# Kernel tuning notes

Hardware: AMD Instinct MI355X
Metric: run time of the kernel (lower is better)

Reference implementation:

```python
import jax, jax.numpy as jnp
import numpy as np

B, L, D = 8, 1024, 1024  # L must equal D for the elementwise sqrt(K) divide to broadcast


def setup_inputs() -> dict:
    key = jax.random.key(0)
    ks = jax.random.split(key, 9)
    # Non-negative inputs/weights/biases so K = x @ Wk.T + bk >= 0 and sqrt(K) is finite.
    rc = jax.random.uniform(ks[0], (B, L, D), dtype=jnp.float32)
    ri = jax.random.uniform(ks[1], (B, L, D), dtype=jnp.float32)
    tc = jax.random.uniform(ks[2], (B, L, D), dtype=jnp.float32)
    scale = 0.02
    Wq = jax.random.uniform(ks[3], (D, D), dtype=jnp.float32) * scale
    Wk = jax.random.uniform(ks[4], (D, D), dtype=jnp.float32) * scale
    Wv = jax.random.uniform(ks[5], (D, D), dtype=jnp.float32) * scale
    bq = jax.random.uniform(ks[6], (D,), dtype=jnp.float32) * scale
    bk = jax.random.uniform(ks[7], (D,), dtype=jnp.float32) * scale
    bv = jax.random.uniform(ks[8], (D,), dtype=jnp.float32) * scale
    return {
        "reference_caption": rc,
        "reference_image": ri,
        "target_caption": tc,
        "Wq": Wq, "bq": bq,
        "Wk": Wk, "bk": bk,
        "Wv": Wv, "bv": bv,
    }


def reference(reference_caption, reference_image, target_caption, Wq, bq, Wk, bk, Wv, bv):
    # torch nn.Linear: y = x @ W.T + b
    Q = reference_caption @ Wq.T + bq          # [B, Lq, D]
    K = reference_image @ Wk.T + bk            # [B, Lk, D]
    V = reference_image @ Wv.T + bv            # [B, Lk, D]
    matmul_qk = jnp.einsum("bqd,bkd->bqk", Q, K)  # [B, Lq, Lk]
    # Faithful to source: elementwise divide by sqrt(K) tensor (broadcasts since Lq==Lk==D).
    scaled_logits = matmul_qk / jnp.sqrt(K)
    attention_weights = jax.nn.softmax(scaled_logits, axis=-1)
    output = jnp.einsum("bqk,bkd->bqd", attention_weights, V)
    return (output, attention_weights)
```

## Files before the change

kernel.cpp:

```cpp
#include <hip/hip_runtime.h>
#include <hip/hip_fp16.h>
#include <math.h>

typedef unsigned short u16;
typedef __attribute__((ext_vector_type(8))) _Float16 half8;
typedef __attribute__((ext_vector_type(4))) float f32x4;

#define ASLOT 4096
#define SLOT  12288

__device__ __forceinline__ u16 f2h(float f){ __half h=__float2half(f); u16 r; __builtin_memcpy(&r,&h,2); return r; }
__device__ __forceinline__ float h2f(u16 u){ __half h; __builtin_memcpy(&h,&u,2); return __half2float(h); }

template<int ROWS>
__device__ __forceinline__ void stage_tile(const u16* __restrict__ G, int rowbase, int ldg,
                                           int k0, u16* Ls, int tid){
#pragma unroll
    for (int p = 0; p < ROWS / 64; ++p){
        const int lin = tid + p * 256;
        const int row = lin >> 2;
        const int cg  = ((lin & 3) ^ ((row >> 1) & 3)) * 8;
        const u16* g = G + (size_t)(rowbase + row) * ldg + (k0 + cg);
        __builtin_amdgcn_global_load_lds(
            (__attribute__((address_space(1))) void*)g,
            (__attribute__((address_space(3))) void*)(Ls + (size_t)lin * 8), 16, 0, 0);
    }
}

template<int EPI, int BIASM>
__device__ __forceinline__ void gemm_core(
    const u16* __restrict__ A, const u16* __restrict__ B,
    const float* __restrict__ bias,
    float* __restrict__ of, u16* __restrict__ oh,
    const float* __restrict__ cm, u16* __restrict__ od,
    int by, int bx, int lda, int ldb, int ldc, int K, u16* sh)
{
    const int tid  = threadIdx.x;
    const int lane = tid & 63, wv = tid >> 6;
    const int wr = (wv >> 1) * 64;
    const int wc = (wv & 1) * 128;
    const int row0 = by * 128, col0 = bx * 256;
    const int lr = lane & 15, hi = lane >> 4;
    const int co = (hi ^ ((lr >> 1) & 3)) * 8;

    f32x4 acc[4][8];
#pragma unroll
    for (int m = 0; m < 4; m++)
#pragma unroll
        for (int n = 0; n < 8; n++) acc[m][n] = (f32x4){0.f, 0.f, 0.f, 0.f};

    auto stage_set = [&](int buf, int k0){
        u16* s = sh + buf * SLOT;
        stage_tile<128>(A, row0, lda, k0, s, tid);
        stage_tile<256>(B, col0, ldb, k0, s + ASLOT, tid);
    };

    const int NIT = K >> 5;
    stage_set(0, 0);
    stage_set(1, 32);
    int bufs = 2, bufr = 0;
    for (int t = 0; t < NIT; ++t){
        if (t + 2 < NIT){ stage_set(bufs, (t + 2) << 5); bufs = (bufs + 1 == 3) ? 0 : bufs + 1; }
        const int rem = NIT - 1 - t;
        if (rem >= 2)      asm volatile("s_waitcnt vmcnt(12)" ::: "memory");
        else if (rem == 1) asm volatile("s_waitcnt vmcnt(6)" ::: "memory");
        else               asm volatile("s_waitcnt vmcnt(0)" ::: "memory");
        __builtin_amdgcn_s_barrier();
        __builtin_amdgcn_sched_barrier(0);

        const u16* s = sh + bufr * SLOT;
        bufr = (bufr + 1 == 3) ? 0 : bufr + 1;

        half8 a[4], b[8];
#pragma unroll
        for (int m = 0; m < 4; m++) a[m] = *(const half8*)&s[(wr + m * 16 + lr) * 32 + co];
#pragma unroll
        for (int n = 0; n < 8; n++) b[n] = *(const half8*)&s[ASLOT + (wc + n * 16 + lr) * 32 + co];
#pragma unroll
        for (int m = 0; m < 4; m++)
#pragma unroll
            for (int n = 0; n < 8; n++)
                acc[m][n] = __builtin_amdgcn_mfma_f32_16x16x32_f16(a[m], b[n], acc[m][n], 0, 0, 0);
        __builtin_amdgcn_sched_barrier(0);
        __builtin_amdgcn_s_barrier();
    }

#pragma unroll
    for (int m = 0; m < 4; m++) {
        const int rb = row0 + wr + m * 16 + hi * 4;
#pragma unroll
        for (int n = 0; n < 8; n++) {
            const int c = col0 + wc + n * 16 + lr;
            const float bc = (BIASM == 1) ? bias[c] : 0.f;
#pragma unroll
            for (int q = 0; q < 4; q++) {
                const int r = rb + q;
                float v = acc[m][n][q] + bc;
                if (BIASM == 2) v += bias[r];
                const size_t idx = (size_t)r * ldc + c;
                if (EPI == 0) of[idx] = v;
                else if (EPI == 1) oh[idx] = f2h(v);
                else {
                    const u16 hh = f2h(v);
                    oh[idx] = hh; oh[idx + 1024] = f2h(v - h2f(hh));
                    if (EPI == 3)
                        od[(size_t)r * 1024 + c] = f2h(v - cm[(size_t)((r >> 10) << 10) + c]);
                }
            }
        }
    }
}

__global__ __launch_bounds__(256, 2) void lin_qk_k(
    const u16* __restrict__ rc_h, const u16* __restrict__ ri_h,
    const u16* __restrict__ Wq_h, const u16* __restrict__ Wk_h,
    const float* __restrict__ bq, const float* __restrict__ bk,
    const float* __restrict__ cm,
    u16* __restrict__ Q_h, u16* __restrict__ Kcat, u16* __restrict__ Kd)
{
    __shared__ __align__(16) u16 sh[3 * SLOT];
    const int nwg = gridDim.x, chunk = nwg >> 3;
    const int swz = ((int)blockIdx.x & 7) * chunk + ((int)blockIdx.x >> 3);
    const int p = swz & 1, t = swz >> 1;
    if (p == 0) {
        gemm_core<1, 1>(rc_h, Wq_h, bq, nullptr, Q_h, nullptr, nullptr,
                        t >> 2, t & 3, 1024, 1024, 1024, 1024, sh);
    } else {
        gemm_core<3, 1>(ri_h, Wk_h, bk, nullptr, Kcat, cm, Kd,
                        t >> 2, t & 3, 1024, 1024, 2048, 1024, sh);
    }
}

__global__ __launch_bounds__(256, 2) void qkt_vt_k(
    const u16* __restrict__ Q_h, const u16* __restrict__ Kd,
    const u16* __restrict__ ri_h, const u16* __restrict__ Wv_h,
    const float* __restrict__ bv, const float* __restrict__ u,
    float* __restrict__ wts, u16* __restrict__ Vt)
{
    __shared__ __align__(16) u16 sh[3 * SLOT];
    const int nwg = gridDim.x, chunk = nwg >> 3;
    const int swz = ((int)blockIdx.x & 7) * chunk + ((int)blockIdx.x >> 3);
    const int p = swz & 1, t = swz >> 1;
    if (p == 0) {
        const int z = t >> 5, rem = t & 31;
        gemm_core<0, 2>(Q_h + ((size_t)z << 20), Kd + ((size_t)z << 20),
                        u + ((size_t)z << 10), wts + ((size_t)z << 20), nullptr,
                        nullptr, nullptr,
                        rem >> 2, rem & 3, 1024, 1024, 1024, 1024, sh);
    } else {
        gemm_core<1, 2>(Wv_h, ri_h, bv, nullptr, Vt, nullptr, nullptr,
                        t >> 5, t & 31, 1024, 1024, 8192, 1024, sh);
    }
}

__global__ __launch_bounds__(256, 2) void av_k(
    const u16* __restrict__ W_h, const u16* __restrict__ Vt, float* __restrict__ outp)
{
    __shared__ __align__(16) u16 sh[3 * SLOT];
    const int nwg = gridDim.x, chunk = nwg >> 3;
    const int wg = ((int)blockIdx.x & 7) * chunk + ((int)blockIdx.x >> 3);
    const int z = wg >> 5, rem = wg & 31;
    gemm_core<0, 0>(W_h + ((size_t)z << 20), Vt + (size_t)z * 1024,
                    nullptr, outp + ((size_t)z << 20), nullptr, nullptr, nullptr,
                    rem >> 2, rem & 3, 1024, 8192, 1024, 1024, sh);
}

__global__ __launch_bounds__(256)
void colmean_k(const u16* __restrict__ ri_h, float* __restrict__ xbar)
{
    const int b = blockIdx.x >> 5, sub = blockIdx.x & 31;
    const int dg = sub & 3, rg = sub >> 2;
    const int d = dg * 256 + threadIdx.x;
    const u16* base = ri_h + ((size_t)b << 20) + ((size_t)(rg * 128) << 10) + d;
    float s = 0.f;
#pragma unroll 4
    for (int r = 0; r < 128; ++r) s += h2f(base[(size_t)r << 10]);
    atomicAdd(&xbar[(b << 10) + d], s * (1.f / 1024.f));
}

template<bool BIAS, bool AFULL>
__global__ __launch_bounds__(256)
void rowdot_k(const u16* __restrict__ A, const float* __restrict__ B,
              const float* __restrict__ bias, float* __restrict__ out)
{
    const int o = blockIdx.x * 4 + (threadIdx.x >> 6);
    const int lane = threadIdx.x & 63;
    const int ar = AFULL ? o : (o & 1023);
    const int br = o >> 10;
    const u16* ap = A + ((size_t)ar << 10);
    const float* bp = B + ((size_t)br << 10);
    float s = 0.f;
#pragma unroll
    for (int j = 0; j < 16; ++j){ const int i = lane + (j << 6); s += h2f(ap[i]) * bp[i]; }
#pragma unroll
    for (int off = 32; off >= 1; off >>= 1) s += __shfl_xor(s, off);
    if (lane == 0) out[o] = s + (BIAS ? bias[ar] : 0.f);
}

__global__ __launch_bounds__(256)
void softmax_scale_k(float* __restrict__ W, const u16* __restrict__ Kcat, u16* __restrict__ Wh)
{
    const long row = blockIdx.x;
    float* p = W + (row << 10);
    const int tid = threadIdx.x;

    float4 v = ((const float4*)p)[tid];
    const ushort4 kh = ((const ushort4*)(Kcat + (row << 11)))[tid];
    const ushort4 kl = ((const ushort4*)(Kcat + (row << 11) + 1024))[tid];
    v.x *= rsqrtf(h2f(kh.x) + h2f(kl.x));
    v.y *= rsqrtf(h2f(kh.y) + h2f(kl.y));
    v.z *= rsqrtf(h2f(kh.z) + h2f(kl.z));
    v.w *= rsqrtf(h2f(kh.w) + h2f(kl.w));

    float m = fmaxf(fmaxf(v.x, v.y), fmaxf(v.z, v.w));
#pragma unroll
    for (int o = 32; o >= 1; o >>= 1) m = fmaxf(m, __shfl_xor(m, o));
    __shared__ float sm[4];
    const int wid = tid >> 6, lane = tid & 63;
    if (lane == 0) sm[wid] = m;
    __syncthreads();
    m = fmaxf(fmaxf(sm[0], sm[1]), fmaxf(sm[2], sm[3]));

    v.x = __expf(v.x - m); v.y = __expf(v.y - m);
    v.z = __expf(v.z - m); v.w = __expf(v.w - m);
    float s = v.x + v.y + v.z + v.w;
#pragma unroll
    for (int o = 32; o >= 1; o >>= 1) s += __shfl_xor(s, o);
    __shared__ float ss[4];
    if (lane == 0) ss[wid] = s;
    __syncthreads();
    s = ss[0] + ss[1] + ss[2] + ss[3];

    const float inv = 1.0f / s;
    v.x *= inv; v.y *= inv; v.z *= inv; v.w *= inv;
    ((float4*)p)[tid] = v;

    ushort4 ub;
    ub.x = f2h(v.x); ub.y = f2h(v.y); ub.z = f2h(v.z); ub.w = f2h(v.w);
    ((ushort4*)(Wh + (row << 10)))[tid] = ub;
}

__global__ __launch_bounds__(256)
void conv_plain5_k(const float4* __restrict__ x0, ushort4* __restrict__ y0,
                   const float4* __restrict__ x1, ushort4* __restrict__ y1,
                   const float4* __restrict__ x2, ushort4* __restrict__ y2,
                   const float4* __restrict__ x3, ushort4* __restrict__ y3,
                   const float4* __restrict__ x4, ushort4* __restrict__ y4)
{
    const long i = (long)blockIdx.x * 256 + threadIdx.x;
    const long n0 = 2097152, n1 = 262144;
    const float4* x; ushort4* y; long j;
    if (i < n0)                 { x = x0; y = y0; j = i; }
    else if (i < 2*n0)          { x = x1; y = y1; j = i - n0; }
    else if (i < 2*n0 + n1)     { x = x2; y = y2; j = i - 2*n0; }
    else if (i < 2*n0 + 2*n1)   { x = x3; y = y3; j = i - 2*n0 - n1; }
    else                        { x = x4; y = y4; j = i - 2*n0 - 2*n1; }
    const float4 v = x[j];
    ushort4 o;
    o.x = f2h(v.x); o.y = f2h(v.y); o.z = f2h(v.z); o.w = f2h(v.w);
    y[j] = o;
}

extern "C" void kernel_launch(void* const* d_in, const int* in_sizes, int n_in,
                              void* d_out, int out_size, void* d_ws, size_t ws_size,
                              hipStream_t stream)
{
    const float* rc = (const float*)d_in[0];
    const float* ri = (const float*)d_in[1];
    const float* Wq = (const float*)d_in[3];
    const float* bq = (const float*)d_in[4];
    const float* Wk = (const float*)d_in[5];
    const float* bk = (const float*)d_in[6];
    const float* Wv = (const float*)d_in[7];
    const float* bv = (const float*)d_in[8];

    const long M8 = 8192 * 1024L;
    const long M1 = 1024 * 1024L;

    u16* ws   = (u16*)d_ws;
    u16* ri_h = ws;
    u16* rc_h = ws + 1 * M8;
    u16* Kcat = ws + 2 * M8;
    u16* Kd   = ws + 4 * M8;
    u16* Wq_h = ws + 5 * M8;
    u16* Wk_h = Wq_h + M1;
    u16* Wv_h = Wk_h + M1;
    float* xbar = (float*)(ws + 5 * M8 + 3 * M1);
    float* cm   = xbar + 8192;
    float* uu   = cm + 8192;

    float* outp = (float*)d_out;
    float* wts  = outp + M8;
    u16*   Q_h  = (u16*)d_out;
    u16*   Vt   = rc_h;
    u16*   W_h  = ri_h;

    conv_plain5_k<<<19456, 256, 0, stream>>>(
        (const float4*)ri, (ushort4*)ri_h, (const float4*)rc, (ushort4*)rc_h,
        (const float4*)Wq, (ushort4*)Wq_h, (const float4*)Wk, (ushort4*)Wk_h,
        (const float4*)Wv, (ushort4*)Wv_h);

    hipMemsetAsync(xbar, 0, 8192 * sizeof(float), stream);
    colmean_k<<<256, 256, 0, stream>>>(ri_h, xbar);

    rowdot_k<true, false><<<2048, 256, 0, stream>>>(Wk_h, xbar, bk, cm);

    lin_qk_k<<<512, 256, 0, stream>>>(rc_h, ri_h, Wq_h, Wk_h, bq, bk, cm, Q_h, Kcat, Kd);

    rowdot_k<false, true><<<2048, 256, 0, stream>>>(Q_h, cm, nullptr, uu);

    qkt_vt_k<<<512, 256, 0, stream>>>(Q_h, Kd, ri_h, Wv_h, bv, uu, wts, Vt);

    softmax_scale_k<<<8192, 256, 0, stream>>>(wts, Kcat, W_h);

    av_k<<<256, 256, 0, stream>>>(W_h, Vt, outp);
}
```

Before: 167.2 us.

## Enlarge GEMM tiles to 256x256 and store K as fp32 instead of split halves

Each GEMM workgroup's tile grows from 128x256 to 256x256, so every wave computes a 128x128 block with 64 accumulators. Grids are halved and launch bounds drop to one block per SM. This raises data reuse per LDS load but costs occupancy, and the smaller grids (128-256 blocks) may underfill the GPU. K is now written as fp32 rather than a hi/lo half pair, which simplifies the softmax scaling read without changing the bytes moved.

```diff
diff --git a/kernel.cpp b/kernel.cpp
--- a/kernel.cpp
+++ b/kernel.cpp
@@ -6,17 +6,16 @@
 typedef __attribute__((ext_vector_type(8))) _Float16 half8;
 typedef __attribute__((ext_vector_type(4))) float f32x4;
 
-#define ASLOT 4096
-#define SLOT  12288
+#define ASLOT 8192
+#define SLOT  16384
 
 __device__ __forceinline__ u16 f2h(float f){ __half h=__float2half(f); u16 r; __builtin_memcpy(&r,&h,2); return r; }
 __device__ __forceinline__ float h2f(u16 u){ __half h; __builtin_memcpy(&h,&u,2); return __half2float(h); }
 
-template<int ROWS>
 __device__ __forceinline__ void stage_tile(const u16* __restrict__ G, int rowbase, int ldg,
                                            int k0, u16* Ls, int tid){
 #pragma unroll
-    for (int p = 0; p < ROWS / 64; ++p){
+    for (int p = 0; p < 4; ++p){
         const int lin = tid + p * 256;
         const int row = lin >> 2;
         const int cg  = ((lin & 3) ^ ((row >> 1) & 3)) * 8;
@@ -37,22 +36,22 @@
 {
     const int tid  = threadIdx.x;
     const int lane = tid & 63, wv = tid >> 6;
-    const int wr = (wv >> 1) * 64;
+    const int wr = (wv >> 1) * 128;
     const int wc = (wv & 1) * 128;
-    const int row0 = by * 128, col0 = bx * 256;
+    const int row0 = by * 256, col0 = bx * 256;
     const int lr = lane & 15, hi = lane >> 4;
     const int co = (hi ^ ((lr >> 1) & 3)) * 8;
 
-    f32x4 acc[4][8];
-#pragma unroll
-    for (int m = 0; m < 4; m++)
+    f32x4 acc[8][8];
+#pragma unroll
+    for (int m = 0; m < 8; m++)
 #pragma unroll
         for (int n = 0; n < 8; n++) acc[m][n] = (f32x4){0.f, 0.f, 0.f, 0.f};
 
     auto stage_set = [&](int buf, int k0){
         u16* s = sh + buf * SLOT;
-        stage_tile<128>(A, row0, lda, k0, s, tid);
-        stage_tile<256>(B, col0, ldb, k0, s + ASLOT, tid);
+        stage_tile(A, row0, lda, k0, s, tid);
+        stage_tile(B, col0, ldb, k0, s + ASLOT, tid);
     };
 
     const int NIT = K >> 5;
@@ -62,8 +61,8 @@
     for (int t = 0; t < NIT; ++t){
         if (t + 2 < NIT){ stage_set(bufs, (t + 2) << 5); bufs = (bufs + 1 == 3) ? 0 : bufs + 1; }
         const int rem = NIT - 1 - t;
-        if (rem >= 2)      asm volatile("s_waitcnt vmcnt(12)" ::: "memory");
-        else if (rem == 1) asm volatile("s_waitcnt vmcnt(6)" ::: "memory");
+        if (rem >= 2)      asm volatile("s_waitcnt vmcnt(16)" ::: "memory");
+        else if (rem == 1) asm volatile("s_waitcnt vmcnt(8)" ::: "memory");
         else               asm volatile("s_waitcnt vmcnt(0)" ::: "memory");
         __builtin_amdgcn_s_barrier();
         __builtin_amdgcn_sched_barrier(0);
@@ -71,13 +70,13 @@
         const u16* s = sh + bufr * SLOT;
         bufr = (bufr + 1 == 3) ? 0 : bufr + 1;
 
-        half8 a[4], b[8];
-#pragma unroll
-        for (int m = 0; m < 4; m++) a[m] = *(const half8*)&s[(wr + m * 16 + lr) * 32 + co];
+        half8 a[8], b[8];
+#pragma unroll
+        for (int m = 0; m < 8; m++) a[m] = *(const half8*)&s[(wr + m * 16 + lr) * 32 + co];
 #pragma unroll
         for (int n = 0; n < 8; n++) b[n] = *(const half8*)&s[ASLOT + (wc + n * 16 + lr) * 32 + co];
 #pragma unroll
-        for (int m = 0; m < 4; m++)
+        for (int m = 0; m < 8; m++)
 #pragma unroll
             for (int n = 0; n < 8; n++)
                 acc[m][n] = __builtin_amdgcn_mfma_f32_16x16x32_f16(a[m], b[n], acc[m][n], 0, 0, 0);
@@ -86,7 +85,7 @@
     }
 
 #pragma unroll
-    for (int m = 0; m < 4; m++) {
+    for (int m = 0; m < 8; m++) {
         const int rb = row0 + wr + m * 16 + hi * 4;
 #pragma unroll
         for (int n = 0; n < 8; n++) {
@@ -101,22 +100,20 @@
                 if (EPI == 0) of[idx] = v;
                 else if (EPI == 1) oh[idx] = f2h(v);
                 else {
-                    const u16 hh = f2h(v);
-                    oh[idx] = hh; oh[idx + 1024] = f2h(v - h2f(hh));
-                    if (EPI == 3)
-                        od[(size_t)r * 1024 + c] = f2h(v - cm[(size_t)((r >> 10) << 10) + c]);
+                    of[idx] = v;
+                    od[idx] = f2h(v - cm[(size_t)((r >> 10) << 10) + c]);
                 }
             }
         }
     }
 }
 
-__global__ __launch_bounds__(256, 2) void lin_qk_k(
+__global__ __launch_bounds__(256, 1) void lin_qk_k(
     const u16* __restrict__ rc_h, const u16* __restrict__ ri_h,
     const u16* __restrict__ Wq_h, const u16* __restrict__ Wk_h,
     const float* __restrict__ bq, const float* __restrict__ bk,
     const float* __restrict__ cm,
-    u16* __restrict__ Q_h, u16* __restrict__ Kcat, u16* __restrict__ Kd)
+    u16* __restrict__ Q_h, float* __restrict__ Kf, u16* __restrict__ Kd)
 {
     __shared__ __align__(16) u16 sh[3 * SLOT];
     const int nwg = gridDim.x, chunk = nwg >> 3;
@@ -126,12 +123,12 @@
         gemm_core<1, 1>(rc_h, Wq_h, bq, nullptr, Q_h, nullptr, nullptr,
                         t >> 2, t & 3, 1024, 1024, 1024, 1024, sh);
     } else {
-        gemm_core<3, 1>(ri_h, Wk_h, bk, nullptr, Kcat, cm, Kd,
-                        t >> 2, t & 3, 1024, 1024, 2048, 1024, sh);
-    }
-}
-
-__global__ __launch_bounds__(256, 2) void qkt_vt_k(
+        gemm_core<3, 1>(ri_h, Wk_h, bk, Kf, nullptr, cm, Kd,
+                        t >> 2, t & 3, 1024, 1024, 1024, 1024, sh);
+    }
+}
+
+__global__ __launch_bounds__(256, 1) void qkt_vt_k(
     const u16* __restrict__ Q_h, const u16* __restrict__ Kd,
     const u16* __restrict__ ri_h, const u16* __restrict__ Wv_h,
     const float* __restrict__ bv, const float* __restrict__ u,
@@ -142,7 +139,7 @@
     const int swz = ((int)blockIdx.x & 7) * chunk + ((int)blockIdx.x >> 3);
     const int p = swz & 1, t = swz >> 1;
     if (p == 0) {
-        const int z = t >> 5, rem = t & 31;
+        const int z = t >> 4, rem = t & 15;
         gemm_core<0, 2>(Q_h + ((size_t)z << 20), Kd + ((size_t)z << 20),
                         u + ((size_t)z << 10), wts + ((size_t)z << 20), nullptr,
                         nullptr, nullptr,
@@ -153,13 +150,13 @@
     }
 }
 
-__global__ __launch_bounds__(256, 2) void av_k(
+__global__ __launch_bounds__(256, 1) void av_k(
     const u16* __restrict__ W_h, const u16* __restrict__ Vt, float* __restrict__ outp)
 {
     __shared__ __align__(16) u16 sh[3 * SLOT];
     const int nwg = gridDim.x, chunk = nwg >> 3;
     const int wg = ((int)blockIdx.x & 7) * chunk + ((int)blockIdx.x >> 3);
-    const int z = wg >> 5, rem = wg & 31;
+    const int z = wg >> 4, rem = wg & 15;
     gemm_core<0, 0>(W_h + ((size_t)z << 20), Vt + (size_t)z * 1024,
                     nullptr, outp + ((size_t)z << 20), nullptr, nullptr, nullptr,
                     rem >> 2, rem & 3, 1024, 8192, 1024, 1024, sh);
@@ -198,19 +195,16 @@
 }
 
 __global__ __launch_bounds__(256)
-void softmax_scale_k(float* __restrict__ W, const u16* __restrict__ Kcat, u16* __restrict__ Wh)
+void softmax_scale_k(float* __restrict__ W, const float* __restrict__ Kf, u16* __restrict__ Wh)
 {
     const long row = blockIdx.x;
     float* p = W + (row << 10);
     const int tid = threadIdx.x;
 
     float4 v = ((const float4*)p)[tid];
-    const ushort4 kh = ((const ushort4*)(Kcat + (row << 11)))[tid];
-    const ushort4 kl = ((const ushort4*)(Kcat + (row << 11) + 1024))[tid];
-    v.x *= rsqrtf(h2f(kh.x) + h2f(kl.x));
-    v.y *= rsqrtf(h2f(kh.y) + h2f(kl.y));
-    v.z *= rsqrtf(h2f(kh.z) + h2f(kl.z));
-    v.w *= rsqrtf(h2f(kh.w) + h2f(kl.w));
+    const float4 kf = ((const float4*)(Kf + (row << 10)))[tid];
+    v.x *= rsqrtf(kf.x); v.y *= rsqrtf(kf.y);
+    v.z *= rsqrtf(kf.z); v.w *= rsqrtf(kf.w);
 
     float m = fmaxf(fmaxf(v.x, v.y), fmaxf(v.z, v.w));
 #pragma unroll
@@ -280,7 +274,7 @@
     u16* ws   = (u16*)d_ws;
     u16* ri_h = ws;
     u16* rc_h = ws + 1 * M8;
-    u16* Kcat = ws + 2 * M8;
+    float* Kf = (float*)(ws + 2 * M8);
     u16* Kd   = ws + 4 * M8;
     u16* Wq_h = ws + 5 * M8;
     u16* Wk_h = Wq_h + M1;
@@ -305,13 +299,13 @@
 
     rowdot_k<true, false><<<2048, 256, 0, stream>>>(Wk_h, xbar, bk, cm);
 
-    lin_qk_k<<<512, 256, 0, stream>>>(rc_h, ri_h, Wq_h, Wk_h, bq, bk, cm, Q_h, Kcat, Kd);
+    lin_qk_k<<<256, 256, 0, stream>>>(rc_h, ri_h, Wq_h, Wk_h, bq, bk, cm, Q_h, Kf, Kd);
 
     rowdot_k<false, true><<<2048, 256, 0, stream>>>(Q_h, cm, nullptr, uu);
 
-    qkt_vt_k<<<512, 256, 0, stream>>>(Q_h, Kd, ri_h, Wv_h, bv, uu, wts, Vt);
-
-    softmax_scale_k<<<8192, 256, 0, stream>>>(wts, Kcat, W_h);
-
-    av_k<<<256, 256, 0, stream>>>(W_h, Vt, outp);
-}
+    qkt_vt_k<<<256, 256, 0, stream>>>(Q_h, Kd, ri_h, Wv_h, bv, uu, wts, Vt);
+
+    softmax_scale_k<<<8192, 256, 0, stream>>>(wts, Kf, W_h);
+
+    av_k<<<128, 256, 0, stream>>>(W_h, Vt, outp);
+}
```

After: 343.7 us. +105.6%, slower.

## Merge Q, K and V projections into one launch and drop hi/lo K storage

Applied to the files above, without the earlier changes.

Computes the V projection together with the Q and K projections in a single three-way launch, and runs QK^T alone in its own launch. The K epilogue now stores the centred value K−cm as fp16 plus a residual, instead of writing both a hi/lo pair of K and a separate centred copy. Softmax rebuilds K from Kd+Krs+cm. This cuts one fp16 K write stream and rebalances grid sizes across the kernels. It needs an extra workspace buffer for Vt and an extra cm read in softmax.

```diff
diff --git a/kernel.cpp b/kernel.cpp
--- a/kernel.cpp
+++ b/kernel.cpp
@@ -101,56 +101,53 @@
                 if (EPI == 0) of[idx] = v;
                 else if (EPI == 1) oh[idx] = f2h(v);
                 else {
-                    const u16 hh = f2h(v);
-                    oh[idx] = hh; oh[idx + 1024] = f2h(v - h2f(hh));
-                    if (EPI == 3)
-                        od[(size_t)r * 1024 + c] = f2h(v - cm[(size_t)((r >> 10) << 10) + c]);
+                    const float d  = v - cm[(size_t)((r >> 10) << 10) + c];
+                    const u16  dh = f2h(d);
+                    oh[idx] = dh;
+                    od[idx] = f2h(d - h2f(dh));
                 }
             }
         }
     }
 }
 
-__global__ __launch_bounds__(256, 2) void lin_qk_k(
+__global__ __launch_bounds__(256, 2) void tri_k(
     const u16* __restrict__ rc_h, const u16* __restrict__ ri_h,
     const u16* __restrict__ Wq_h, const u16* __restrict__ Wk_h,
+    const u16* __restrict__ Wv_h,
     const float* __restrict__ bq, const float* __restrict__ bk,
-    const float* __restrict__ cm,
-    u16* __restrict__ Q_h, u16* __restrict__ Kcat, u16* __restrict__ Kd)
+    const float* __restrict__ bv, const float* __restrict__ cm,
+    u16* __restrict__ Q_h, u16* __restrict__ Kd, u16* __restrict__ Krs,
+    u16* __restrict__ Vt)
 {
     __shared__ __align__(16) u16 sh[3 * SLOT];
     const int nwg = gridDim.x, chunk = nwg >> 3;
     const int swz = ((int)blockIdx.x & 7) * chunk + ((int)blockIdx.x >> 3);
-    const int p = swz & 1, t = swz >> 1;
+    const int p = swz % 3, t = swz / 3;
     if (p == 0) {
         gemm_core<1, 1>(rc_h, Wq_h, bq, nullptr, Q_h, nullptr, nullptr,
                         t >> 2, t & 3, 1024, 1024, 1024, 1024, sh);
-    } else {
-        gemm_core<3, 1>(ri_h, Wk_h, bk, nullptr, Kcat, cm, Kd,
-                        t >> 2, t & 3, 1024, 1024, 2048, 1024, sh);
-    }
-}
-
-__global__ __launch_bounds__(256, 2) void qkt_vt_k(
-    const u16* __restrict__ Q_h, const u16* __restrict__ Kd,
-    const u16* __restrict__ ri_h, const u16* __restrict__ Wv_h,
-    const float* __restrict__ bv, const float* __restrict__ u,
-    float* __restrict__ wts, u16* __restrict__ Vt)
-{
-    __shared__ __align__(16) u16 sh[3 * SLOT];
-    const int nwg = gridDim.x, chunk = nwg >> 3;
-    const int swz = ((int)blockIdx.x & 7) * chunk + ((int)blockIdx.x >> 3);
-    const int p = swz & 1, t = swz >> 1;
-    if (p == 0) {
-        const int z = t >> 5, rem = t & 31;
-        gemm_core<0, 2>(Q_h + ((size_t)z << 20), Kd + ((size_t)z << 20),
-                        u + ((size_t)z << 10), wts + ((size_t)z << 20), nullptr,
-                        nullptr, nullptr,
-                        rem >> 2, rem & 3, 1024, 1024, 1024, 1024, sh);
+    } else if (p == 1) {
+        gemm_core<5, 1>(ri_h, Wk_h, bk, nullptr, Kd, cm, Krs,
+                        t >> 2, t & 3, 1024, 1024, 1024, 1024, sh);
     } else {
         gemm_core<1, 2>(Wv_h, ri_h, bv, nullptr, Vt, nullptr, nullptr,
                         t >> 5, t & 31, 1024, 1024, 8192, 1024, sh);
     }
+}
+
+__global__ __launch_bounds__(256, 2) void qkt_k(
+    const u16* __restrict__ Q_h, const u16* __restrict__ Kd,
+    const float* __restrict__ u, float* __restrict__ wts)
+{
+    __shared__ __align__(16) u16 sh[3 * SLOT];
+    const int nwg = gridDim.x, chunk = nwg >> 3;
+    const int swz = ((int)blockIdx.x & 7) * chunk + ((int)blockIdx.x >> 3);
+    const int z = swz >> 5, rem = swz & 31;
+    gemm_core<0, 2>(Q_h + ((size_t)z << 20), Kd + ((size_t)z << 20),
+                    u + ((size_t)z << 10), wts + ((size_t)z << 20), nullptr,
+                    nullptr, nullptr,
+                    rem >> 2, rem & 3, 1024, 1024, 1024, 1024, sh);
 }
 
 __global__ __launch_bounds__(256, 2) void av_k(
@@ -198,19 +195,23 @@
 }
 
 __global__ __launch_bounds__(256)
-void softmax_scale_k(float* __restrict__ W, const u16* __restrict__ Kcat, u16* __restrict__ Wh)
+void softmax_scale_k(float* __restrict__ W, const u16* __restrict__ Kd,
+                     const u16* __restrict__ Krs, const float* __restrict__ cm,
+                     u16* __restrict__ Wh)
 {
     const long row = blockIdx.x;
+    const int b = (int)(row >> 10);
     float* p = W + (row << 10);
     const int tid = threadIdx.x;
 
     float4 v = ((const float4*)p)[tid];
-    const ushort4 kh = ((const ushort4*)(Kcat + (row << 11)))[tid];
-    const ushort4 kl = ((const ushort4*)(Kcat + (row << 11) + 1024))[tid];
-    v.x *= rsqrtf(h2f(kh.x) + h2f(kl.x));
-    v.y *= rsqrtf(h2f(kh.y) + h2f(kl.y));
-    v.z *= rsqrtf(h2f(kh.z) + h2f(kl.z));
-    v.w *= rsqrtf(h2f(kh.w) + h2f(kl.w));
+    const ushort4 kd = ((const ushort4*)(Kd + (row << 10)))[tid];
+    const ushort4 ks = ((const ushort4*)(Krs + (row << 10)))[tid];
+    const float4 cmv = ((const float4*)(cm + ((size_t)b << 10)))[tid];
+    v.x *= rsqrtf(h2f(kd.x) + h2f(ks.x) + cmv.x);
+    v.y *= rsqrtf(h2f(kd.y) + h2f(ks.y) + cmv.y);
+    v.z *= rsqrtf(h2f(kd.z) + h2f(ks.z) + cmv.z);
+    v.w *= rsqrtf(h2f(kd.w) + h2f(ks.w) + cmv.w);
 
     float m = fmaxf(fmaxf(v.x, v.y), fmaxf(v.z, v.w));
 #pragma unroll
@@ -280,8 +281,9 @@
     u16* ws   = (u16*)d_ws;
     u16* ri_h = ws;
     u16* rc_h = ws + 1 * M8;
-    u16* Kcat = ws + 2 * M8;
-    u16* Kd   = ws + 4 * M8;
+    u16* Kd   = ws + 2 * M8;
+    u16* Krs  = ws + 3 * M8;
+    u16* Vt   = ws + 4 * M8;
     u16* Wq_h = ws + 5 * M8;
     u16* Wk_h = Wq_h + M1;
     u16* Wv_h = Wk_h + M1;
@@ -292,7 +294,6 @@
     float* outp = (float*)d_out;
     float* wts  = outp + M8;
     u16*   Q_h  = (u16*)d_out;
-    u16*   Vt   = rc_h;
     u16*   W_h  = ri_h;
 
     conv_plain5_k<<<19456, 256, 0, stream>>>(
@@ -305,13 +306,14 @@
 
     rowdot_k<true, false><<<2048, 256, 0, stream>>>(Wk_h, xbar, bk, cm);
 
-    lin_qk_k<<<512, 256, 0, stream>>>(rc_h, ri_h, Wq_h, Wk_h, bq, bk, cm, Q_h, Kcat, Kd);
+    tri_k<<<768, 256, 0, stream>>>(rc_h, ri_h, Wq_h, Wk_h, Wv_h,
+                                   bq, bk, bv, cm, Q_h, Kd, Krs, Vt);
 
     rowdot_k<false, true><<<2048, 256, 0, stream>>>(Q_h, cm, nullptr, uu);
 
-    qkt_vt_k<<<512, 256, 0, stream>>>(Q_h, Kd, ri_h, Wv_h, bv, uu, wts, Vt);
-
-    softmax_scale_k<<<8192, 256, 0, stream>>>(wts, Kcat, W_h);
+    qkt_k<<<256, 256, 0, stream>>>(Q_h, Kd, uu, wts);
+
+    softmax_scale_k<<<8192, 256, 0, stream>>>(wts, Kd, Krs, cm, W_h);
 
     av_k<<<256, 256, 0, stream>>>(W_h, Vt, outp);
 }
```

Measured after the change: 174.4 us. 1.04x slower.
